# Performance work log

Measured on AMD Instinct MI355X. Metric: run time of the kernel, lower is better.

The kernel has to match this reference:

```python
import jax, jax.numpy as jnp
import numpy as np

T = 200                      # TRAIN_ROIS_PER_IMAGE
RATIO = 0.33                 # ROI_POSITIVE_RATIO
P_MAX = int(T * RATIO)       # max positive ROIs (66)
MH, MW = 28, 28              # MASK_SHAPE
STD = jnp.array([0.1, 0.1, 0.2, 0.2], jnp.float32)  # BBOX_STD_DEV
EPS = 1e-6


def _iou(a, b):
    # a [N,4], b [G,4] -> [N,G] IoU (same math as overlaps_graph, without tiling)
    ay1, ax1, ay2, ax2 = a[:, 0:1], a[:, 1:2], a[:, 2:3], a[:, 3:4]
    by1, bx1, by2, bx2 = b[None, :, 0], b[None, :, 1], b[None, :, 2], b[None, :, 3]
    iy = jnp.maximum(jnp.minimum(ay2, by2) - jnp.maximum(ay1, by1), 0.0)
    ix = jnp.maximum(jnp.minimum(ax2, bx2) - jnp.maximum(ax1, bx1), 0.0)
    inter = iy * ix
    union = (ay2 - ay1) * (ax2 - ax1) + (by2 - by1) * (bx2 - bx1) - inter
    return inter / jnp.maximum(union, EPS)


def _box_refinement(box, gt):
    # standard Mask R-CNN box_refinement_graph
    h = jnp.maximum(box[:, 2] - box[:, 0], EPS)
    w = jnp.maximum(box[:, 3] - box[:, 1], EPS)
    cy = box[:, 0] + 0.5 * h
    cx = box[:, 1] + 0.5 * w
    gh = jnp.maximum(gt[:, 2] - gt[:, 0], EPS)
    gw = jnp.maximum(gt[:, 3] - gt[:, 1], EPS)
    gcy = gt[:, 0] + 0.5 * gh
    gcx = gt[:, 1] + 0.5 * gw
    return jnp.stack([(gcy - cy) / h, (gcx - cx) / w,
                      jnp.log(gh / h), jnp.log(gw / w)], axis=-1)


def _crop_and_resize(imgs, boxes):
    # imgs [T,H,W], boxes [T,4] normalized; TF crop_and_resize bilinear semantics,
    # extrapolation_value = 0 for samples outside [0, H-1] x [0, W-1].
    Tn, H, W = imgs.shape
    y1, x1, y2, x2 = boxes[:, 0], boxes[:, 1], boxes[:, 2], boxes[:, 3]
    iy = jnp.arange(MH, dtype=jnp.float32)
    ix = jnp.arange(MW, dtype=jnp.float32)
    ys = y1[:, None] * (H - 1) + iy[None, :] * ((y2 - y1) * (H - 1) / (MH - 1))[:, None]  # [T,MH]
    xs = x1[:, None] * (W - 1) + ix[None, :] * ((x2 - x1) * (W - 1) / (MW - 1))[:, None]  # [T,MW]
    y0 = jnp.floor(ys); x0 = jnp.floor(xs)
    wy = (ys - y0)[:, :, None]
    wx = (xs - x0)[:, None, :]
    y0i = jnp.clip(y0, 0, H - 1).astype(jnp.int32)
    y1i = jnp.clip(y0 + 1, 0, H - 1).astype(jnp.int32)
    x0i = jnp.clip(x0, 0, W - 1).astype(jnp.int32)
    x1i = jnp.clip(x0 + 1, 0, W - 1).astype(jnp.int32)
    t = jnp.arange(Tn)[:, None, None]
    v00 = imgs[t, y0i[:, :, None], x0i[:, None, :]]
    v01 = imgs[t, y0i[:, :, None], x1i[:, None, :]]
    v10 = imgs[t, y1i[:, :, None], x0i[:, None, :]]
    v11 = imgs[t, y1i[:, :, None], x1i[:, None, :]]
    val = (v00 * (1 - wx) + v01 * wx) * (1 - wy) + (v10 * (1 - wx) + v11 * wx) * wy
    ok = ((ys >= 0) & (ys <= H - 1))[:, :, None] & ((xs >= 0) & (xs <= W - 1))[:, None, :]
    return jnp.where(ok, val, 0.0)


def _targets_one(proposals, class_ids, boxes, masks):
    # proposals [N,4], class_ids [G] int, boxes [G,4], masks [H,W,G]
    N = proposals.shape[0]
    # zero-padding trim expressed as validity masks (jit-friendly fixed shapes)
    valid_prop = jnp.any(proposals != 0, axis=1)
    valid_gt = jnp.any(boxes != 0, axis=1)
    non_crowd = (class_ids > 0) & valid_gt
    crowd = (class_ids < 0) & valid_gt

    ov = _iou(proposals, boxes)                              # [N,G]
    ov_nc = jnp.where(non_crowd[None, :], ov, -1.0)          # mask crowd/padded gt
    roi_iou_max = ov_nc.max(axis=1)
    crowd_max = jnp.where(crowd[None, :], ov, 0.0).max(axis=1)

    pos_mask = valid_prop & (roi_iou_max >= 0.5)
    neg_mask = valid_prop & (roi_iou_max < 0.5) & (crowd_max < 0.001)

    # deterministic selection (original uses tf.random.shuffle): positives first-in-order
    pos_order = jnp.argsort(jnp.where(pos_mask, 0, 1))
    neg_order = jnp.argsort(jnp.where(neg_mask, 0, 1))
    pos_count = jnp.minimum(pos_mask.sum(), P_MAX)
    neg_needed = jnp.floor(pos_count.astype(jnp.float32) / RATIO).astype(jnp.int32) - pos_count
    neg_count = jnp.minimum(jnp.minimum(neg_needed, neg_mask.sum()), T - pos_count)

    slot = jnp.arange(T)
    is_pos = slot < pos_count
    is_neg = (slot >= pos_count) & (slot < pos_count + neg_count)
    src = jnp.where(is_pos,
                    pos_order[jnp.clip(slot, 0, N - 1)],
                    neg_order[jnp.clip(slot - pos_count, 0, N - 1)])
    rois = jnp.where((is_pos | is_neg)[:, None], proposals[src], 0.0)

    assign = jnp.argmax(ov_nc[src], axis=1)                  # gt assignment per slot
    gt_box = boxes[assign]
    gt_cls = jnp.where(is_pos, class_ids[assign], 0)

    deltas = _box_refinement(rois, gt_box) / STD
    deltas = jnp.where(is_pos[:, None], deltas, 0.0)

    # USE_MINI_MASK: roi box in gt-box-normalized coordinates
    gy1, gx1, gy2, gx2 = gt_box[:, 0], gt_box[:, 1], gt_box[:, 2], gt_box[:, 3]
    gh = jnp.maximum(gy2 - gy1, EPS)
    gw = jnp.maximum(gx2 - gx1, EPS)
    mm = jnp.stack([(rois[:, 0] - gy1) / gh, (rois[:, 1] - gx1) / gw,
                    (rois[:, 2] - gy1) / gh, (rois[:, 3] - gx1) / gw], axis=-1)

    roi_masks = jnp.moveaxis(jnp.take(masks, assign, axis=2), 2, 0)  # [T,H,W]
    m = jnp.round(_crop_and_resize(roi_masks, mm))
    m = jnp.where(is_pos[:, None, None], m, 0.0)
    return rois, gt_cls, deltas, m


def setup_inputs() -> dict:
    key = jax.random.key(0)
    ks = jax.random.split(key, 4)
    B, N, G, HM = 16, 2000, 200, 56

    def boxes_of(k, shape):
        k1, k2, k3, k4 = jax.random.split(k, 4)
        y1 = jax.random.uniform(k1, shape) * 0.5
        x1 = jax.random.uniform(k2, shape) * 0.5
        h = 0.1 + jax.random.uniform(k3, shape) * 0.4
        w = 0.1 + jax.random.uniform(k4, shape) * 0.4
        return jnp.stack([y1, x1, y1 + h, x1 + w], axis=-1)

    proposals = boxes_of(ks[0], (B, N))
    proposals = proposals * (jnp.arange(N) < N - 200)[None, :, None]  # zero-padded tail
    prior_class_ids = jax.random.randint(ks[1], (B, G), -1, 81).astype(jnp.int32)  # -1=crowd, 0=padding
    prior_boxes = boxes_of(ks[2], (B, G)) * (prior_class_ids != 0)[..., None]
    prior_masks = (jax.random.uniform(ks[3], (B, HM, HM, G)) > 0.5).astype(jnp.float32)
    return {"proposals": proposals, "prior_class_ids": prior_class_ids,
            "prior_boxes": prior_boxes, "prior_masks": prior_masks}


def reference(proposals, prior_class_ids, prior_boxes, prior_masks):
    rois, cls, deltas, masks = jax.vmap(_targets_one)(proposals, prior_class_ids,
                                                      prior_boxes, prior_masks)
    return rois, cls, deltas, masks
```

## Files before the change

kernel.cpp:

```cpp
#include <hip/hip_runtime.h>
#include <math.h>

#pragma clang fp contract(off)

#define BN    16
#define NP    2000
#define NG    200
#define NT    200
#define PMAX  66
#define EPSF  1e-6f
#define MH    28
#define MW    28
#define HM    56
#define NPIX  (HM*HM)
#define NSLOT 128

__global__ __launch_bounds__(256) void kA(
    const float* __restrict__ proposals, const int* __restrict__ cls_ids,
    const float* __restrict__ boxes,
    int* __restrict__ flag_ws, int* __restrict__ assign_ws)
{
#pragma clang fp contract(off)
  const int b = blockIdx.y;
  __shared__ float4 gbox[NG];
  __shared__ float  garea[NG];
  __shared__ int    gflag[NG];

  for (int j = threadIdx.x; j < NG; j += 256) {
    float4 g = reinterpret_cast<const float4*>(boxes + (size_t)b * NG * 4)[j];
    int c = cls_ids[b * NG + j];
    bool vg = (g.x != 0.f) || (g.y != 0.f) || (g.z != 0.f) || (g.w != 0.f);
    gbox[j]  = g;
    garea[j] = (g.z - g.x) * (g.w - g.y);
    gflag[j] = vg ? (c > 0 ? 1 : (c < 0 ? 2 : 0)) : 0;
  }
  __syncthreads();

  int i = blockIdx.x * 256 + threadIdx.x;
  if (i >= NP) return;

  float4 p = reinterpret_cast<const float4*>(proposals + (size_t)b * NP * 4)[i];
  bool vp = (p.x != 0.f) || (p.y != 0.f) || (p.z != 0.f) || (p.w != 0.f);
  float pa = (p.z - p.x) * (p.w - p.y);

  float best = -3.0e38f;
  int   bestj = 0;
  float cmax = 0.f;
  for (int j = 0; j < NG; ++j) {
    float4 g = gbox[j];
    float iy = fmaxf(fminf(p.z, g.z) - fmaxf(p.x, g.x), 0.f);
    float ix = fmaxf(fminf(p.w, g.w) - fmaxf(p.y, g.y), 0.f);
    float inter = iy * ix;
    float uni = (pa + garea[j]) - inter;
    float iou = inter / fmaxf(uni, EPSF);
    int fl = gflag[j];
    float v = (fl == 1) ? iou : -1.0f;
    if (v > best) { best = v; bestj = j; }
    if (fl == 2) cmax = fmaxf(cmax, iou);
  }
  bool pos = vp && (best >= 0.5f);
  bool neg = vp && (best < 0.5f) && (cmax < 0.001f);
  flag_ws[b * NP + i]   = pos ? 1 : (neg ? 2 : 0);
  assign_ws[b * NP + i] = bestj;
}

__global__ __launch_bounds__(256) void kB(
    const float* __restrict__ proposals, const int* __restrict__ cls_ids,
    const float* __restrict__ boxes, const int* __restrict__ flag_ws,
    const int* __restrict__ assign_ws, float* __restrict__ out,
    float* __restrict__ mm_ws, int* __restrict__ ma_ws)
{
#pragma clang fp contract(off)
  const int b = blockIdx.x;
  const int tid = threadIdx.x;
  const int lane = tid & 63;
  const int wv = tid >> 6;

  __shared__ unsigned short pos_list[NP];
  __shared__ unsigned short neg_list[NP];
  __shared__ int wcp[4], wcn[4];
  __shared__ int s_pt, s_nt;
  if (tid == 0) { s_pt = 0; s_nt = 0; }
  __syncthreads();

  const int* fb = flag_ws + b * NP;
  for (int base = 0; base < NP; base += 256) {
    int i = base + tid;
    int f = (i < NP) ? fb[i] : 0;
    bool isp = (f == 1), isn = (f == 2);
    unsigned long long bp = __ballot(isp);
    unsigned long long bn = __ballot(isn);
    __syncthreads();
    if (lane == 0) { wcp[wv] = __popcll(bp); wcn[wv] = __popcll(bn); }
    __syncthreads();
    int prep = __popcll(bp & ((1ull << lane) - 1ull));
    int pren = __popcll(bn & ((1ull << lane) - 1ull));
    int bpp = 0, bnn = 0, tp = 0, tn = 0;
    for (int w = 0; w < 4; ++w) {
      if (w < wv) { bpp += wcp[w]; bnn += wcn[w]; }
      tp += wcp[w]; tn += wcn[w];
    }
    int pt = s_pt, nt = s_nt;
    if (isp) pos_list[pt + bpp + prep] = (unsigned short)i;
    if (isn) neg_list[nt + bnn + pren] = (unsigned short)i;
    __syncthreads();
    if (tid == 0) { s_pt = pt + tp; s_nt = nt + tn; }
  }
  __syncthreads();

  int pos_total = s_pt, neg_total = s_nt;
  int pos_count = min(pos_total, PMAX);
  int neg_needed = (int)floorf((float)pos_count / 0.33f) - pos_count;
  int neg_count = min(min(neg_needed, neg_total), NT - pos_count);

  if (tid < NT) {
    bool ispos = tid < pos_count;
    bool isneg = (!ispos) && (tid < pos_count + neg_count);
    float r0 = 0.f, r1 = 0.f, r2 = 0.f, r3 = 0.f;
    float d0 = 0.f, d1 = 0.f, d2 = 0.f, d3 = 0.f;
    float m0 = 0.f, m1 = 0.f, m2 = 0.f, m3 = 0.f;
    float clsf = 0.f;
    int ma = -1;
    if (ispos || isneg) {
      int i = ispos ? (int)pos_list[tid] : (int)neg_list[tid - pos_count];
      float4 p = reinterpret_cast<const float4*>(proposals + (size_t)b * NP * 4)[i];
      r0 = p.x; r1 = p.y; r2 = p.z; r3 = p.w;
      if (ispos) {
        int a = assign_ws[b * NP + i];
        ma = a;
        float4 g = reinterpret_cast<const float4*>(boxes + (size_t)b * NG * 4)[a];
        float h  = fmaxf(r2 - r0, EPSF);
        float w  = fmaxf(r3 - r1, EPSF);
        float cy = r0 + 0.5f * h;
        float cx = r1 + 0.5f * w;
        float gh = fmaxf(g.z - g.x, EPSF);
        float gw = fmaxf(g.w - g.y, EPSF);
        float gcy = g.x + 0.5f * gh;
        float gcx = g.y + 0.5f * gw;
        d0 = ((gcy - cy) / h) / 0.1f;
        d1 = ((gcx - cx) / w) / 0.1f;
        d2 = logf(gh / h) / 0.2f;
        d3 = logf(gw / w) / 0.2f;
        m0 = (r0 - g.x) / gh;
        m1 = (r1 - g.y) / gw;
        m2 = (r2 - g.x) / gh;
        m3 = (r3 - g.y) / gw;
        clsf = (float)cls_ids[b * NG + a];
      }
    }
    int s = b * NT + tid;
    float* rois = out;
    float* cls  = out + BN * NT * 4;
    float* dlt  = out + BN * NT * 4 + BN * NT;
    rois[s * 4 + 0] = r0; rois[s * 4 + 1] = r1;
    rois[s * 4 + 2] = r2; rois[s * 4 + 3] = r3;
    cls[s] = clsf;
    dlt[s * 4 + 0] = d0; dlt[s * 4 + 1] = d1;
    dlt[s * 4 + 2] = d2; dlt[s * 4 + 3] = d3;
    mm_ws[s * 4 + 0] = m0; mm_ws[s * 4 + 1] = m1;
    mm_ws[s * 4 + 2] = m2; mm_ws[s * 4 + 3] = m3;
    ma_ws[s] = ma;
  }
}

__global__ __launch_bounds__(256) void kG(
    const float* __restrict__ masks, const int* __restrict__ ma_ws,
    float* __restrict__ staged)
{
  const int b  = blockIdx.z;
  const int s0 = blockIdx.y * 64;
  const int p0 = blockIdx.x * 64;
  __shared__ float tile[64][65];
  __shared__ int   sma[64];
  const int tid = threadIdx.x;
  if (tid < 64) sma[tid] = ma_ws[b * NT + s0 + tid];
  __syncthreads();

  const float* mbase = masks + (size_t)b * NPIX * NG;
  for (int e = 0; e < 16; ++e) {
    int idx = e * 256 + tid;
    int sl  = idx & 63;
    int pl  = idx >> 6;
    int g   = sma[sl];
    float v = 0.f;
    if (g >= 0) v = mbase[(size_t)(p0 + pl) * NG + g];
    tile[sl][pl] = v;
  }
  __syncthreads();
  for (int e = 0; e < 16; ++e) {
    int idx = e * 256 + tid;
    int pl  = idx & 63;
    int sl  = idx >> 6;
    if (sma[sl] >= 0)
      staged[(size_t)(b * NSLOT + s0 + sl) * NPIX + (p0 + pl)] = tile[sl][pl];
  }
}

__global__ __launch_bounds__(256) void kC(
    const float* __restrict__ staged, const float* __restrict__ mm_ws,
    const int* __restrict__ ma_ws, float* __restrict__ out)
{
#pragma clang fp contract(off)
  const int s = blockIdx.x;
  float4* om = reinterpret_cast<float4*>(
      out + (size_t)(BN * NT * 9) + (size_t)s * (MH * MW));
  const int q = threadIdx.x;
  if (q >= (MH * MW) / 4) return;
  int a = ma_ws[s];
  if (a < 0) { om[q] = make_float4(0.f, 0.f, 0.f, 0.f); return; }

  const int b = s / NT;
  const int t = s - b * NT;
  float y1 = mm_ws[s * 4 + 0], x1 = mm_ws[s * 4 + 1];
  float y2 = mm_ws[s * 4 + 2], x2 = mm_ws[s * 4 + 3];
  float sy = (y2 - y1) * 55.0f / 27.0f;
  float sx = (x2 - x1) * 55.0f / 27.0f;
  const float* mp = staged + (size_t)(b * NSLOT + t) * NPIX;

  int px0 = q * 4;
  int my  = px0 / MW;
  float ys = y1 * 55.0f + (float)my * sy;
  float y0f = floorf(ys);
  float wy  = ys - y0f;
  int y0i = (int)fminf(fmaxf(y0f, 0.f), 55.f);
  int y1i = (int)fminf(fmaxf(y0f + 1.0f, 0.f), 55.f);
  bool oky = (ys >= 0.f) && (ys <= 55.f);
  const float* r0 = mp + y0i * HM;
  const float* r1 = mp + y1i * HM;

  float res[4];
  for (int k = 0; k < 4; ++k) {
    int mx = (px0 + k) - my * MW;
    float xs = x1 * 55.0f + (float)mx * sx;
    float x0f = floorf(xs);
    float wx  = xs - x0f;
    int x0i = (int)fminf(fmaxf(x0f, 0.f), 55.f);
    int x1i = (int)fminf(fmaxf(x0f + 1.0f, 0.f), 55.f);
    float v00 = r0[x0i], v01 = r0[x1i];
    float v10 = r1[x0i], v11 = r1[x1i];
    float val = (v00 * (1.f - wx) + v01 * wx) * (1.f - wy)
              + (v10 * (1.f - wx) + v11 * wx) * wy;
    bool ok = oky && (xs >= 0.f) && (xs <= 55.f);
    res[k] = ok ? rintf(val) : 0.f;
  }
  om[q] = make_float4(res[0], res[1], res[2], res[3]);
}

extern "C" void kernel_launch(void* const* d_in, const int* in_sizes, int n_in,
                              void* d_out, int out_size, void* d_ws, size_t ws_size,
                              hipStream_t stream)
{
  const float* proposals = (const float*)d_in[0];
  const int*   cls_ids   = (const int*)d_in[1];
  const float* boxes     = (const float*)d_in[2];
  const float* masks     = (const float*)d_in[3];
  float* out = (float*)d_out;

  char* ws = (char*)d_ws;
  int*   flag_ws   = (int*)ws;    ws += (size_t)BN * NP * sizeof(int);
  int*   assign_ws = (int*)ws;    ws += (size_t)BN * NP * sizeof(int);
  float* mm_ws     = (float*)ws;  ws += (size_t)BN * NT * 4 * sizeof(float);
  int*   ma_ws     = (int*)ws;    ws += (size_t)BN * NT * sizeof(int);
  float* staged    = (float*)ws;

  dim3 gA((NP + 255) / 256, BN);
  kA<<<gA, 256, 0, stream>>>(proposals, cls_ids, boxes, flag_ws, assign_ws);
  kB<<<BN, 256, 0, stream>>>(proposals, cls_ids, boxes, flag_ws, assign_ws,
                             out, mm_ws, ma_ws);
  dim3 gG(NPIX / 64, NSLOT / 64, BN);
  kG<<<gG, 256, 0, stream>>>(masks, ma_ws, staged);
  kC<<<BN * NT, 256, 0, stream>>>(staged, mm_ws, ma_ws, out);
}
```

Before: 129.4 us.

## Stage masks per unique assigned GT instead of per positive ROI slot

kB now marks which GT instances are used by positive ROIs, compacts them into plane indices, and writes a GT-to-plane map plus a per-ROI plane index. kG walks GT columns in chunks of 64 and reads contiguous mask rows, transposes them, and writes only the used GT planes, skipping chunks with no used GT. kC reads from the deduplicated planes. The aim is to replace the scattered per-slot gathers with contiguous row reads and to cut staged writes when several ROIs share a GT. The cost is that kG may now read all 200 columns per pixel tile, and its grid is smaller with a serial loop over chunks.

```diff
diff --git a/kernel.cpp b/kernel.cpp
--- a/kernel.cpp
+++ b/kernel.cpp
@@ -3,17 +3,17 @@
 
 #pragma clang fp contract(off)
 
-#define BN    16
-#define NP    2000
-#define NG    200
-#define NT    200
-#define PMAX  66
-#define EPSF  1e-6f
-#define MH    28
-#define MW    28
-#define HM    56
-#define NPIX  (HM*HM)
-#define NSLOT 128
+#define BN     16
+#define NP     2000
+#define NG     200
+#define NT     200
+#define PMAX   66
+#define EPSF   1e-6f
+#define MH     28
+#define MW     28
+#define HM     56
+#define NPIX   (HM*HM)
+#define NPLANE 66
 
 __global__ __launch_bounds__(256) void kA(
     const float* __restrict__ proposals, const int* __restrict__ cls_ids,
@@ -68,7 +68,8 @@
     const float* __restrict__ proposals, const int* __restrict__ cls_ids,
     const float* __restrict__ boxes, const int* __restrict__ flag_ws,
     const int* __restrict__ assign_ws, float* __restrict__ out,
-    float* __restrict__ mm_ws, int* __restrict__ ma_ws)
+    float* __restrict__ mm_ws, int* __restrict__ pa_ws,
+    int* __restrict__ gmap_ws)
 {
 #pragma clang fp contract(off)
   const int b = blockIdx.x;
@@ -80,6 +81,9 @@
   __shared__ unsigned short neg_list[NP];
   __shared__ int wcp[4], wcn[4];
   __shared__ int s_pt, s_nt;
+  __shared__ int used[NG];
+  __shared__ int gplane[NG];
+  __shared__ int wtot[4];
   if (tid == 0) { s_pt = 0; s_nt = 0; }
   __syncthreads();
 
@@ -113,6 +117,10 @@
   int neg_needed = (int)floorf((float)pos_count / 0.33f) - pos_count;
   int neg_count = min(min(neg_needed, neg_total), NT - pos_count);
 
+  for (int j = tid; j < NG; j += 256) used[j] = 0;
+  __syncthreads();
+
+  int ma = -1;
   if (tid < NT) {
     bool ispos = tid < pos_count;
     bool isneg = (!ispos) && (tid < pos_count + neg_count);
@@ -120,7 +128,6 @@
     float d0 = 0.f, d1 = 0.f, d2 = 0.f, d3 = 0.f;
     float m0 = 0.f, m1 = 0.f, m2 = 0.f, m3 = 0.f;
     float clsf = 0.f;
-    int ma = -1;
     if (ispos || isneg) {
       int i = ispos ? (int)pos_list[tid] : (int)neg_list[tid - pos_count];
       float4 p = reinterpret_cast<const float4*>(proposals + (size_t)b * NP * 4)[i];
@@ -128,6 +135,7 @@
       if (ispos) {
         int a = assign_ws[b * NP + i];
         ma = a;
+        used[a] = 1;
         float4 g = reinterpret_cast<const float4*>(boxes + (size_t)b * NG * 4)[a];
         float h  = fmaxf(r2 - r0, EPSF);
         float w  = fmaxf(r3 - r1, EPSF);
@@ -159,46 +167,77 @@
     dlt[s * 4 + 2] = d2; dlt[s * 4 + 3] = d3;
     mm_ws[s * 4 + 0] = m0; mm_ws[s * 4 + 1] = m1;
     mm_ws[s * 4 + 2] = m2; mm_ws[s * 4 + 3] = m3;
-    ma_ws[s] = ma;
-  }
+  }
+  __syncthreads();
+
+  {
+    int j = tid;
+    int u = (j < NG) ? used[j] : 0;
+    unsigned long long m = __ballot(u != 0);
+    int pre = __popcll(m & ((1ull << lane) - 1ull));
+    if (lane == 0) wtot[wv] = __popcll(m);
+    __syncthreads();
+    int basep = 0;
+    for (int w = 0; w < wv; ++w) basep += wtot[w];
+    if (j < NG) {
+      int pl = u ? (basep + pre) : -1;
+      gplane[j] = pl;
+      gmap_ws[b * NG + j] = pl;
+    }
+  }
+  __syncthreads();
+
+  if (tid < NT)
+    pa_ws[b * NT + tid] = (ma >= 0) ? gplane[ma] : -1;
 }
 
 __global__ __launch_bounds__(256) void kG(
-    const float* __restrict__ masks, const int* __restrict__ ma_ws,
+    const float* __restrict__ masks, const int* __restrict__ gmap_ws,
     float* __restrict__ staged)
 {
-  const int b  = blockIdx.z;
-  const int s0 = blockIdx.y * 64;
+  const int b  = blockIdx.y;
   const int p0 = blockIdx.x * 64;
+  const int tid = threadIdx.x;
   __shared__ float tile[64][65];
-  __shared__ int   sma[64];
-  const int tid = threadIdx.x;
-  if (tid < 64) sma[tid] = ma_ws[b * NT + s0 + tid];
-  __syncthreads();
+  __shared__ int   splane[64];
+  __shared__ int   s_any;
 
   const float* mbase = masks + (size_t)b * NPIX * NG;
-  for (int e = 0; e < 16; ++e) {
-    int idx = e * 256 + tid;
-    int sl  = idx & 63;
-    int pl  = idx >> 6;
-    int g   = sma[sl];
-    float v = 0.f;
-    if (g >= 0) v = mbase[(size_t)(p0 + pl) * NG + g];
-    tile[sl][pl] = v;
-  }
-  __syncthreads();
-  for (int e = 0; e < 16; ++e) {
-    int idx = e * 256 + tid;
-    int pl  = idx & 63;
-    int sl  = idx >> 6;
-    if (sma[sl] >= 0)
-      staged[(size_t)(b * NSLOT + s0 + sl) * NPIX + (p0 + pl)] = tile[sl][pl];
+
+  for (int gc = 0; gc < NG; gc += 64) {
+    if (tid < 64)
+      splane[tid] = (gc + tid < NG) ? gmap_ws[b * NG + gc + tid] : -1;
+    if (tid == 0) s_any = 0;
+    __syncthreads();
+    if (tid < 64 && splane[tid] >= 0) s_any = 1;
+    __syncthreads();
+    if (s_any) {
+      for (int e = 0; e < 16; ++e) {
+        int idx = e * 256 + tid;
+        int gl  = idx & 63;
+        int pl  = idx >> 6;
+        int g   = gc + gl;
+        float v = 0.f;
+        if (g < NG) v = mbase[(size_t)(p0 + pl) * NG + g];
+        tile[gl][pl] = v;
+      }
+      __syncthreads();
+      for (int e = 0; e < 16; ++e) {
+        int idx = e * 256 + tid;
+        int pl  = idx & 63;
+        int gl  = idx >> 6;
+        int plane = splane[gl];
+        if (plane >= 0)
+          staged[(size_t)(b * NPLANE + plane) * NPIX + (p0 + pl)] = tile[gl][pl];
+      }
+    }
+    __syncthreads();
   }
 }
 
 __global__ __launch_bounds__(256) void kC(
     const float* __restrict__ staged, const float* __restrict__ mm_ws,
-    const int* __restrict__ ma_ws, float* __restrict__ out)
+    const int* __restrict__ pa_ws, float* __restrict__ out)
 {
 #pragma clang fp contract(off)
   const int s = blockIdx.x;
@@ -206,16 +245,15 @@
       out + (size_t)(BN * NT * 9) + (size_t)s * (MH * MW));
   const int q = threadIdx.x;
   if (q >= (MH * MW) / 4) return;
-  int a = ma_ws[s];
-  if (a < 0) { om[q] = make_float4(0.f, 0.f, 0.f, 0.f); return; }
+  int pa = pa_ws[s];
+  if (pa < 0) { om[q] = make_float4(0.f, 0.f, 0.f, 0.f); return; }
 
   const int b = s / NT;
-  const int t = s - b * NT;
   float y1 = mm_ws[s * 4 + 0], x1 = mm_ws[s * 4 + 1];
   float y2 = mm_ws[s * 4 + 2], x2 = mm_ws[s * 4 + 3];
   float sy = (y2 - y1) * 55.0f / 27.0f;
   float sx = (x2 - x1) * 55.0f / 27.0f;
-  const float* mp = staged + (size_t)(b * NSLOT + t) * NPIX;
+  const float* mp = staged + (size_t)(b * NPLANE + pa) * NPIX;
 
   int px0 = q * 4;
   int my  = px0 / MW;
@@ -260,14 +298,15 @@
   int*   flag_ws   = (int*)ws;    ws += (size_t)BN * NP * sizeof(int);
   int*   assign_ws = (int*)ws;    ws += (size_t)BN * NP * sizeof(int);
   float* mm_ws     = (float*)ws;  ws += (size_t)BN * NT * 4 * sizeof(float);
-  int*   ma_ws     = (int*)ws;    ws += (size_t)BN * NT * sizeof(int);
+  int*   pa_ws     = (int*)ws;    ws += (size_t)BN * NT * sizeof(int);
+  int*   gmap_ws   = (int*)ws;    ws += (size_t)BN * NG * sizeof(int);
   float* staged    = (float*)ws;
 
   dim3 gA((NP + 255) / 256, BN);
   kA<<<gA, 256, 0, stream>>>(proposals, cls_ids, boxes, flag_ws, assign_ws);
   kB<<<BN, 256, 0, stream>>>(proposals, cls_ids, boxes, flag_ws, assign_ws,
-                             out, mm_ws, ma_ws);
-  dim3 gG(NPIX / 64, NSLOT / 64, BN);
-  kG<<<gG, 256, 0, stream>>>(masks, ma_ws, staged);
-  kC<<<BN * NT, 256, 0, stream>>>(staged, mm_ws, ma_ws, out);
-}
+                             out, mm_ws, pa_ws, gmap_ws);
+  dim3 gG(NPIX / 64, BN);
+  kG<<<gG, 256, 0, stream>>>(masks, gmap_ws, staged);
+  kC<<<BN * NT, 256, 0, stream>>>(staged, mm_ws, pa_ws, out);
+}
```

Result: slower. 140.1 us (+8.3%).
